# Optimization experiments

Measured on AMD Instinct MI355X. Metric: run time of the kernel, lower is better.

The kernel has to match this reference:

```python
import jax, jax.numpy as jnp
import numpy as np

N, IN_CH, OUT_CH = 2, 16, 32
SPATIAL = (20, 20, 20, 20)
KER = (3, 3, 3, 3)


def setup_inputs() -> dict:
    key = jax.random.key(0)
    kx, kw = jax.random.split(key)
    x = jax.random.normal(kx, (N, IN_CH) + SPATIAL, dtype=jnp.float32)
    # kaiming-uniform-like init scale; exact init distribution irrelevant for correctness baseline
    fan_in = IN_CH * int(np.prod(KER))
    bound = float(np.sqrt(6.0 / fan_in))
    w = jax.random.uniform(kw, (IN_CH, OUT_CH) + KER, dtype=jnp.float32,
                           minval=-bound, maxval=bound)
    return {"x": x, "w": w}


def reference(x, w):
    # x: [n, in_ch, d1, d2, d3, d4]; w: [in_ch, out_ch, k1, k2, k3, k4]
    # valid 4D convolution (cross-correlation), stride 1 -- same math as the
    # torch as_strided im2col + tensordot, but expressed as a sum over the
    # (small, fixed) kernel offsets to avoid materializing the im2col tensor.
    kd = w.shape[2:]
    od = tuple(x.shape[2 + i] - kd[i] + 1 for i in range(4))  # output spatial dims
    out = jnp.zeros((x.shape[0], w.shape[1]) + od, dtype=x.dtype)
    for a in range(kd[0]):
        for b in range(kd[1]):
            for c in range(kd[2]):
                for d in range(kd[3]):
                    patch = x[:, :, a:a + od[0], b:b + od[1], c:c + od[2], d:d + od[3]]
                    out = out + jnp.einsum('ncijkl,co->noijkl', patch, w[:, :, a, b, c, d])
    return out
```

## Files before the change

kernel.cpp:

```cpp
#include <hip/hip_runtime.h>


typedef unsigned short ushort_t;
typedef __attribute__((ext_vector_type(8)))  __bf16 bf16x8;
typedef __attribute__((ext_vector_type(16))) float  f32x16;
typedef __attribute__((ext_vector_type(4)))  unsigned int uint4v;

__device__ __forceinline__ ushort_t f2bf(float f) {
    union { float f; unsigned int u; } v; v.f = f;
    unsigned int r = v.u + 0x7FFFu + ((v.u >> 16) & 1u);
    return (ushort_t)(r >> 16);
}

__device__ __forceinline__ void gload16(const ushort_t* g, ushort_t* l) {
    __builtin_amdgcn_global_load_lds(
        (const __attribute__((address_space(1))) unsigned int*)g,
        (__attribute__((address_space(3))) unsigned int*)l, 16, 0, 0);
}

__global__ __launch_bounds__(256) void prepass(const float* __restrict__ x,
                                               const float* __restrict__ w,
                                               ushort_t* __restrict__ xt,
                                               ushort_t* __restrict__ wt) {
    const int blk = blockIdx.x;
    if (blk < 1250) {
        const int g = blk * 256 + threadIdx.x;
        const int n = g / 160000, rem = g % 160000;
        const float* xs = x + (size_t)n * 2560000 + rem;
        unsigned int pk[8];
        #pragma unroll
        for (int e = 0; e < 8; ++e) {
            unsigned int lo = f2bf(xs[(size_t)(2 * e) * 160000]);
            unsigned int hi = f2bf(xs[(size_t)(2 * e + 1) * 160000]);
            pk[e] = lo | (hi << 16);
        }
        uint4v* q = (uint4v*)xt + (size_t)g * 2;
        uint4v q0; q0[0] = pk[0]; q0[1] = pk[1]; q0[2] = pk[2]; q0[3] = pk[3];
        uint4v q1; q1[0] = pk[4]; q1[1] = pk[5]; q1[2] = pk[6]; q1[3] = pk[7];
        q[0] = q0; q[1] = q1;
    } else {
        const int s = (blk - 1250) * 256 + threadIdx.x;
        if (s < 41472) {
            const int ic = s / 2592, rem = s % 2592;
            const int oc = rem / 81, tap = rem % 81;
            wt[tap * 512 + oc * 16 + ic] = f2bf(w[s]);
        }
    }
}

__global__ __launch_bounds__(256, 2) void conv4d_mfma(
    const ushort_t* __restrict__ xt, const ushort_t* __restrict__ wt,
    float* __restrict__ out)
{
    __shared__ ushort_t lx[2][6400];
    __shared__ float edgebuf[4][3][2][16];

    const int wgid = blockIdx.x;
    const int tile_ = (wgid & 7) * 81 + (wgid >> 3);
    const int n = tile_ / 324;
    const int rem_ = tile_ - n * 324;
    const int j = rem_ / 18, i = rem_ % 18;

    const int t = threadIdx.x;
    const int lane = t & 63, wv = t >> 6;
    const int col = lane & 31, ic8 = lane >> 5;

    int sp[3]; int cb[3];
    #pragma unroll
    for (int m = 0; m < 3; ++m) {
        sp[m] = (3 * wv + m) * 32 + col;
        const int spc = sp[m] > 359 ? 359 : sp[m];
        cb[m] = spc * 32 + ic8 * 16;
    }

    f32x16 acc[3][3];
    #pragma unroll
    for (int d = 0; d < 3; ++d)
        #pragma unroll
        for (int m = 0; m < 3; ++m)
            #pragma unroll
            for (int r = 0; r < 16; ++r) acc[d][m][r] = 0.0f;

    const ushort_t* xbase = xt + (size_t)n * 2560000;

    {
        const ushort_t* g = xbase + (size_t)i * 128000 + (size_t)j * 6400;
        ushort_t* l0 = lx[0] + (wv << 9);
        const ushort_t* gt = g + t * 8;
        gload16(gt,          l0);
        gload16(gt + 2048,   l0 + 2048);
        gload16(gt + 4096,   l0 + 4096);
        if (t < 32) gload16(g + 6144 + t * 8, lx[0] + 6144);
    }

    int cur = 0;
    for (int ab = 0; ab < 9; ++ab) {
        __syncthreads();

        if (ab < 8) {
            const int a = (ab + 1) / 3, b = (ab + 1) % 3;
            const ushort_t* g = xbase + (size_t)(i + a) * 128000 + (size_t)(j + b) * 6400;
            ushort_t* lb = lx[cur ^ 1];
            ushort_t* l0 = lb + (wv << 9);
            const ushort_t* gt = g + t * 8;
            gload16(gt,          l0);
            gload16(gt + 2048,   l0 + 2048);
            gload16(gt + 4096,   l0 + 4096);
            if (t < 32) gload16(g + 6144 + t * 8, lb + 6144);
        }

        const char* lbase = (const char*)lx[cur];
        #pragma unroll
        for (int c = 0; c < 3; ++c) {
            const ushort_t* wtb = wt + (size_t)(ab * 9 + c * 3) * 512 + col * 16 + ic8 * 8;
            bf16x8 af0 = *(const bf16x8*)(wtb);
            bf16x8 af1 = *(const bf16x8*)(wtb + 512);
            bf16x8 af2 = *(const bf16x8*)(wtb + 1024);
            #pragma unroll
            for (int m = 0; m < 3; ++m) {
                bf16x8 bv = *(const bf16x8*)(lbase + cb[m] + c * 640);
                acc[0][m] = __builtin_amdgcn_mfma_f32_32x32x16_bf16(af0, bv, acc[0][m], 0, 0, 0);
                acc[1][m] = __builtin_amdgcn_mfma_f32_32x32x16_bf16(af1, bv, acc[1][m], 0, 0, 0);
                acc[2][m] = __builtin_amdgcn_mfma_f32_32x32x16_bf16(af2, bv, acc[2][m], 0, 0, 0);
            }
        }

        if (ab < 8) cur ^= 1;
    }

    if (col == 0) {
        #pragma unroll
        for (int r = 0; r < 16; ++r) {
            edgebuf[wv][0][ic8][r] = acc[1][0][r];
            edgebuf[wv][1][ic8][r] = acc[2][0][r];
        }
    } else if (col == 1) {
        #pragma unroll
        for (int r = 0; r < 16; ++r)
            edgebuf[wv][2][ic8][r] = acc[2][0][r];
    }
    __syncthreads();
    const int nw = wv < 3 ? wv + 1 : 3;

    bool valm[3]; float* po[3];
    float* outn = out + (size_t)n * 3359232 + (size_t)i * 5832 + (size_t)j * 324
                      + (size_t)ic8 * 419904;
    #pragma unroll
    for (int m = 0; m < 3; ++m) {
        const int s = sp[m];
        const int k = s / 20, ls = s % 20;
        valm[m] = (ls <= 17) && (s <= 357);
        po[m] = outn + k * 18 + ls;
    }
    const int src1 = (lane & 32) | ((col + 1) & 31);
    const int src2 = (lane & 32) | ((col + 2) & 31);

    #pragma unroll
    for (int r = 0; r < 16; ++r) {
        const float e1  = edgebuf[nw][0][ic8][r];
        const float e2a = edgebuf[nw][1][ic8][r];
        const float e2b = edgebuf[nw][2][ic8][r];
        float t1[4], t2[4];
        #pragma unroll
        for (int m = 0; m < 3; ++m) {
            t1[m] = __shfl(acc[1][m][r], src1, 64);
            t2[m] = __shfl(acc[2][m][r], src2, 64);
        }
        t1[3] = e1;
        t2[3] = (col == 30) ? e2a : e2b;
        const int offr = ((r & 3) + 8 * (r >> 2)) * 104976;
        #pragma unroll
        for (int m = 0; m < 3; ++m) {
            const float v1 = (col == 31) ? t1[m + 1] : t1[m];
            const float v2 = (col >= 30) ? t2[m + 1] : t2[m];
            const float res = acc[0][m][r] + v1 + v2;
            if (valm[m]) po[m][offr] = res;
        }
    }
}

extern "C" void kernel_launch(void* const* d_in, const int* in_sizes, int n_in,
                              void* d_out, int out_size, void* d_ws, size_t ws_size,
                              hipStream_t stream) {
    const float* x = (const float*)d_in[0];
    const float* w = (const float*)d_in[1];
    float* out = (float*)d_out;

    ushort_t* xt = (ushort_t*)d_ws;
    ushort_t* wt = (ushort_t*)((char*)d_ws + (size_t)10240000);

    prepass<<<dim3(1412), 256, 0, stream>>>(x, w, xt, wt);
    conv4d_mfma<<<dim3(648), 256, 0, stream>>>(xt, wt, out);
}
```

Before: 48.81 us.

## Fuse fp32-to-bf16 input transpose into conv kernel with swizzled LDS staging

Removes the separate pass that converted x to a channel-last bf16 copy in workspace. The conv kernel now loads fp32 x directly into registers, converts and packs it to bf16, and writes it to an XOR-swizzled LDS layout while the MFMAs on the previous buffer run. All nine weight fragments per iteration are also loaded up front. This drops the extra global write and read of the converted input, but costs more registers, redoes the conversion in every block that touches overlapping rows, and gives up async global-to-LDS loads.

```diff
diff --git a/kernel.cpp b/kernel.cpp
--- a/kernel.cpp
+++ b/kernel.cpp
@@ -12,44 +12,18 @@
     return (ushort_t)(r >> 16);
 }
 
-__device__ __forceinline__ void gload16(const ushort_t* g, ushort_t* l) {
-    __builtin_amdgcn_global_load_lds(
-        (const __attribute__((address_space(1))) unsigned int*)g,
-        (__attribute__((address_space(3))) unsigned int*)l, 16, 0, 0);
-}
-
-__global__ __launch_bounds__(256) void prepass(const float* __restrict__ x,
-                                               const float* __restrict__ w,
-                                               ushort_t* __restrict__ xt,
-                                               ushort_t* __restrict__ wt) {
-    const int blk = blockIdx.x;
-    if (blk < 1250) {
-        const int g = blk * 256 + threadIdx.x;
-        const int n = g / 160000, rem = g % 160000;
-        const float* xs = x + (size_t)n * 2560000 + rem;
-        unsigned int pk[8];
-        #pragma unroll
-        for (int e = 0; e < 8; ++e) {
-            unsigned int lo = f2bf(xs[(size_t)(2 * e) * 160000]);
-            unsigned int hi = f2bf(xs[(size_t)(2 * e + 1) * 160000]);
-            pk[e] = lo | (hi << 16);
-        }
-        uint4v* q = (uint4v*)xt + (size_t)g * 2;
-        uint4v q0; q0[0] = pk[0]; q0[1] = pk[1]; q0[2] = pk[2]; q0[3] = pk[3];
-        uint4v q1; q1[0] = pk[4]; q1[1] = pk[5]; q1[2] = pk[6]; q1[3] = pk[7];
-        q[0] = q0; q[1] = q1;
-    } else {
-        const int s = (blk - 1250) * 256 + threadIdx.x;
-        if (s < 41472) {
-            const int ic = s / 2592, rem = s % 2592;
-            const int oc = rem / 81, tap = rem % 81;
-            wt[tap * 512 + oc * 16 + ic] = f2bf(w[s]);
-        }
-    }
-}
-
-__global__ __launch_bounds__(256, 2) void conv4d_mfma(
-    const ushort_t* __restrict__ xt, const ushort_t* __restrict__ wt,
+__global__ __launch_bounds__(256) void prep_w(const float* __restrict__ w,
+                                              ushort_t* __restrict__ wt) {
+    int s = blockIdx.x * 256 + threadIdx.x;
+    if (s < 41472) {
+        int ic = s / 2592, rem = s % 2592;
+        int oc = rem / 81, tap = rem % 81;
+        wt[tap * 512 + oc * 16 + ic] = f2bf(w[s]);
+    }
+}
+
+__global__ __launch_bounds__(256, 2) void conv4d_fused(
+    const float* __restrict__ x, const ushort_t* __restrict__ wt,
     float* __restrict__ out)
 {
     __shared__ ushort_t lx[2][6400];
@@ -81,51 +55,84 @@
             #pragma unroll
             for (int r = 0; r < 16; ++r) acc[d][m][r] = 0.0f;
 
-    const ushort_t* xbase = xt + (size_t)n * 2560000;
-
-    {
-        const ushort_t* g = xbase + (size_t)i * 128000 + (size_t)j * 6400;
-        ushort_t* l0 = lx[0] + (wv << 9);
-        const ushort_t* gt = g + t * 8;
-        gload16(gt,          l0);
-        gload16(gt + 2048,   l0 + 2048);
-        gload16(gt + 4096,   l0 + 4096);
-        if (t < 32) gload16(g + 6144 + t * 8, lx[0] + 6144);
+    const float* xn = x + (size_t)n * 2560000;
+    const bool stg = (t < 200);
+    const int p0 = 2 * t;
+    const int wlog = 64 * t;
+    const int wphys = wlog ^ (((wlog >> 7) & 7) << 4);
+
+    float2 val[16];
+
+    if (stg) {
+        const float* xr = xn + (size_t)i * 8000 + (size_t)j * 400 + p0;
+        #pragma unroll
+        for (int ic = 0; ic < 16; ++ic)
+            val[ic] = *(const float2*)(xr + (size_t)ic * 160000);
+        char* base = (char*)lx[0];
+        uint4v c0, c1, c2, c3;
+        #pragma unroll
+        for (int m = 0; m < 4; ++m) {
+            c0[m] = (unsigned)f2bf(val[2*m].x)     | ((unsigned)f2bf(val[2*m+1].x) << 16);
+            c1[m] = (unsigned)f2bf(val[2*m+8].x)   | ((unsigned)f2bf(val[2*m+9].x) << 16);
+            c2[m] = (unsigned)f2bf(val[2*m].y)     | ((unsigned)f2bf(val[2*m+1].y) << 16);
+            c3[m] = (unsigned)f2bf(val[2*m+8].y)   | ((unsigned)f2bf(val[2*m+9].y) << 16);
+        }
+        *(uint4v*)(base + (wphys ^ 0))  = c0;
+        *(uint4v*)(base + (wphys ^ 16)) = c1;
+        *(uint4v*)(base + (wphys ^ 32)) = c2;
+        *(uint4v*)(base + (wphys ^ 48)) = c3;
     }
 
     int cur = 0;
     for (int ab = 0; ab < 9; ++ab) {
         __syncthreads();
 
-        if (ab < 8) {
+        bf16x8 af[9];
+        const ushort_t* wtb = wt + (size_t)(ab * 9) * 512 + col * 16 + ic8 * 8;
+        #pragma unroll
+        for (int cd = 0; cd < 9; ++cd)
+            af[cd] = *(const bf16x8*)(wtb + cd * 512);
+
+        if (ab < 8 && stg) {
             const int a = (ab + 1) / 3, b = (ab + 1) % 3;
-            const ushort_t* g = xbase + (size_t)(i + a) * 128000 + (size_t)(j + b) * 6400;
-            ushort_t* lb = lx[cur ^ 1];
-            ushort_t* l0 = lb + (wv << 9);
-            const ushort_t* gt = g + t * 8;
-            gload16(gt,          l0);
-            gload16(gt + 2048,   l0 + 2048);
-            gload16(gt + 4096,   l0 + 4096);
-            if (t < 32) gload16(g + 6144 + t * 8, lb + 6144);
+            const float* xr = xn + (size_t)(i + a) * 8000 + (size_t)(j + b) * 400 + p0;
+            #pragma unroll
+            for (int ic = 0; ic < 16; ++ic)
+                val[ic] = *(const float2*)(xr + (size_t)ic * 160000);
         }
 
         const char* lbase = (const char*)lx[cur];
         #pragma unroll
         for (int c = 0; c < 3; ++c) {
-            const ushort_t* wtb = wt + (size_t)(ab * 9 + c * 3) * 512 + col * 16 + ic8 * 8;
-            bf16x8 af0 = *(const bf16x8*)(wtb);
-            bf16x8 af1 = *(const bf16x8*)(wtb + 512);
-            bf16x8 af2 = *(const bf16x8*)(wtb + 1024);
             #pragma unroll
             for (int m = 0; m < 3; ++m) {
-                bf16x8 bv = *(const bf16x8*)(lbase + cb[m] + c * 640);
-                acc[0][m] = __builtin_amdgcn_mfma_f32_32x32x16_bf16(af0, bv, acc[0][m], 0, 0, 0);
-                acc[1][m] = __builtin_amdgcn_mfma_f32_32x32x16_bf16(af1, bv, acc[1][m], 0, 0, 0);
-                acc[2][m] = __builtin_amdgcn_mfma_f32_32x32x16_bf16(af2, bv, acc[2][m], 0, 0, 0);
+                const int lg = cb[m] + c * 640;
+                const int ph = lg ^ (((lg >> 7) & 7) << 4);
+                bf16x8 bv = *(const bf16x8*)(lbase + ph);
+                acc[0][m] = __builtin_amdgcn_mfma_f32_32x32x16_bf16(af[c*3+0], bv, acc[0][m], 0, 0, 0);
+                acc[1][m] = __builtin_amdgcn_mfma_f32_32x32x16_bf16(af[c*3+1], bv, acc[1][m], 0, 0, 0);
+                acc[2][m] = __builtin_amdgcn_mfma_f32_32x32x16_bf16(af[c*3+2], bv, acc[2][m], 0, 0, 0);
             }
         }
 
-        if (ab < 8) cur ^= 1;
+        if (ab < 8) {
+            if (stg) {
+                char* base = (char*)lx[cur ^ 1];
+                uint4v c0, c1, c2, c3;
+                #pragma unroll
+                for (int m = 0; m < 4; ++m) {
+                    c0[m] = (unsigned)f2bf(val[2*m].x)   | ((unsigned)f2bf(val[2*m+1].x) << 16);
+                    c1[m] = (unsigned)f2bf(val[2*m+8].x) | ((unsigned)f2bf(val[2*m+9].x) << 16);
+                    c2[m] = (unsigned)f2bf(val[2*m].y)   | ((unsigned)f2bf(val[2*m+1].y) << 16);
+                    c3[m] = (unsigned)f2bf(val[2*m+8].y) | ((unsigned)f2bf(val[2*m+9].y) << 16);
+                }
+                *(uint4v*)(base + (wphys ^ 0))  = c0;
+                *(uint4v*)(base + (wphys ^ 16)) = c1;
+                *(uint4v*)(base + (wphys ^ 32)) = c2;
+                *(uint4v*)(base + (wphys ^ 48)) = c3;
+            }
+            cur ^= 1;
+        }
     }
 
     if (col == 0) {
@@ -186,9 +193,8 @@
     const float* w = (const float*)d_in[1];
     float* out = (float*)d_out;
 
-    ushort_t* xt = (ushort_t*)d_ws;
-    ushort_t* wt = (ushort_t*)((char*)d_ws + (size_t)10240000);
-
-    prepass<<<dim3(1412), 256, 0, stream>>>(x, w, xt, wt);
-    conv4d_mfma<<<dim3(648), 256, 0, stream>>>(xt, wt, out);
-}
+    ushort_t* wt = (ushort_t*)d_ws;
+
+    prep_w<<<dim3(162), 256, 0, stream>>>(w, wt);
+    conv4d_fused<<<dim3(648), 256, 0, stream>>>(x, wt, out);
+}
```

After: 48.79 us. Within noise of the previous version (-0.0%).

## Load all nine input slabs into LDS upfront and drop double buffering

Applied to the files above, without the earlier changes.

Replaces the two-slot double-buffered LDS pipeline with a single upfront issue of all nine (a,b) input slabs into a large shared buffer, then one barrier before the MFMA loop. This removes the per-iteration __syncthreads and keeps all global loads in flight together. In exchange LDS use grows to about 115 KB per block and launch bounds drop to one block per SM, which lowers occupancy and leaves no compute to overlap with the initial load wait.

```diff
diff --git a/kernel.cpp b/kernel.cpp
--- a/kernel.cpp
+++ b/kernel.cpp
@@ -48,12 +48,12 @@
     }
 }
 
-__global__ __launch_bounds__(256, 2) void conv4d_mfma(
+__global__ __launch_bounds__(256, 1) void conv4d_mfma(
     const ushort_t* __restrict__ xt, const ushort_t* __restrict__ wt,
     float* __restrict__ out)
 {
-    __shared__ ushort_t lx[2][6400];
-    __shared__ float edgebuf[4][3][2][16];
+    __shared__ ushort_t smem[57600];
+    __shared__ float edge[384];
 
     const int wgid = blockIdx.x;
     const int tile_ = (wgid & 7) * 81 + (wgid >> 3);
@@ -83,39 +83,29 @@
 
     const ushort_t* xbase = xt + (size_t)n * 2560000;
 
-    {
-        const ushort_t* g = xbase + (size_t)i * 128000 + (size_t)j * 6400;
-        ushort_t* l0 = lx[0] + (wv << 9);
+    #pragma unroll
+    for (int s9 = 0; s9 < 9; ++s9) {
+        const int a = s9 / 3, b = s9 % 3;
+        const ushort_t* g = xbase + (size_t)(i + a) * 128000 + (size_t)(j + b) * 6400;
+        ushort_t* l = smem + s9 * 6400;
+        ushort_t* l0 = l + (wv << 9);
         const ushort_t* gt = g + t * 8;
-        gload16(gt,          l0);
-        gload16(gt + 2048,   l0 + 2048);
-        gload16(gt + 4096,   l0 + 4096);
-        if (t < 32) gload16(g + 6144 + t * 8, lx[0] + 6144);
+        gload16(gt,        l0);
+        gload16(gt + 2048, l0 + 2048);
+        gload16(gt + 4096, l0 + 4096);
+        if (t < 32) gload16(g + 6144 + t * 8, l + 6144);
     }
+    __syncthreads();
 
-    int cur = 0;
+    #pragma unroll 3
     for (int ab = 0; ab < 9; ++ab) {
-        __syncthreads();
-
-        if (ab < 8) {
-            const int a = (ab + 1) / 3, b = (ab + 1) % 3;
-            const ushort_t* g = xbase + (size_t)(i + a) * 128000 + (size_t)(j + b) * 6400;
-            ushort_t* lb = lx[cur ^ 1];
-            ushort_t* l0 = lb + (wv << 9);
-            const ushort_t* gt = g + t * 8;
-            gload16(gt,          l0);
-            gload16(gt + 2048,   l0 + 2048);
-            gload16(gt + 4096,   l0 + 4096);
-            if (t < 32) gload16(g + 6144 + t * 8, lb + 6144);
-        }
-
-        const char* lbase = (const char*)lx[cur];
+        const ushort_t* wtb = wt + (size_t)ab * 4608 + col * 16 + ic8 * 8;
+        const char* lbase = (const char*)(smem + ab * 6400);
         #pragma unroll
         for (int c = 0; c < 3; ++c) {
-            const ushort_t* wtb = wt + (size_t)(ab * 9 + c * 3) * 512 + col * 16 + ic8 * 8;
-            bf16x8 af0 = *(const bf16x8*)(wtb);
-            bf16x8 af1 = *(const bf16x8*)(wtb + 512);
-            bf16x8 af2 = *(const bf16x8*)(wtb + 1024);
+            bf16x8 af0 = *(const bf16x8*)(wtb + (c * 3 + 0) * 512);
+            bf16x8 af1 = *(const bf16x8*)(wtb + (c * 3 + 1) * 512);
+            bf16x8 af2 = *(const bf16x8*)(wtb + (c * 3 + 2) * 512);
             #pragma unroll
             for (int m = 0; m < 3; ++m) {
                 bf16x8 bv = *(const bf16x8*)(lbase + cb[m] + c * 640);
@@ -124,20 +114,18 @@
                 acc[2][m] = __builtin_amdgcn_mfma_f32_32x32x16_bf16(af2, bv, acc[2][m], 0, 0, 0);
             }
         }
-
-        if (ab < 8) cur ^= 1;
     }
 
     if (col == 0) {
         #pragma unroll
         for (int r = 0; r < 16; ++r) {
-            edgebuf[wv][0][ic8][r] = acc[1][0][r];
-            edgebuf[wv][1][ic8][r] = acc[2][0][r];
+            edge[((wv * 3 + 0) * 2 + ic8) * 16 + r] = acc[1][0][r];
+            edge[((wv * 3 + 1) * 2 + ic8) * 16 + r] = acc[2][0][r];
         }
     } else if (col == 1) {
         #pragma unroll
         for (int r = 0; r < 16; ++r)
-            edgebuf[wv][2][ic8][r] = acc[2][0][r];
+            edge[((wv * 3 + 2) * 2 + ic8) * 16 + r] = acc[2][0][r];
     }
     __syncthreads();
     const int nw = wv < 3 ? wv + 1 : 3;
@@ -157,9 +145,9 @@
 
     #pragma unroll
     for (int r = 0; r < 16; ++r) {
-        const float e1  = edgebuf[nw][0][ic8][r];
-        const float e2a = edgebuf[nw][1][ic8][r];
-        const float e2b = edgebuf[nw][2][ic8][r];
+        const float e1  = edge[((nw * 3 + 0) * 2 + ic8) * 16 + r];
+        const float e2a = edge[((nw * 3 + 1) * 2 + ic8) * 16 + r];
+        const float e2b = edge[((nw * 3 + 2) * 2 + ic8) * 16 + r];
         float t1[4], t2[4];
         #pragma unroll
         for (int m = 0; m < 3; ++m) {
@@ -171,9 +159,9 @@
         const int offr = ((r & 3) + 8 * (r >> 2)) * 104976;
         #pragma unroll
         for (int m = 0; m < 3; ++m) {
-            const float v1 = (col == 31) ? t1[m + 1] : t1[m];
-            const float v2 = (col >= 30) ? t2[m + 1] : t2[m];
-            const float res = acc[0][m][r] + v1 + v2;
+            const float v1m = (col == 31) ? t1[m + 1] : t1[m];
+            const float v2m = (col >= 30) ? t2[m + 1] : t2[m];
+            const float res = acc[0][m][r] + v1m + v2m;
             if (valm[m]) po[m][offr] = res;
         }
     }
```

Result: slower. 57.21 us (+17.2%).
